# Kernel optimization log

Hardware: AMD Instinct MI355X
Metric: run time of the kernel (lower is better)

Reference implementation:

```python
import jax, jax.numpy as jnp
import numpy as np

N, H, V = 4096, 1024, 16384


def setup_inputs() -> dict:
    key = jax.random.key(0)
    k1, k2, k3, k4 = jax.random.split(key, 4)
    _input = jax.random.normal(k1, (N, H), dtype=jnp.float32)
    weight = jax.random.normal(k2, (V, H), dtype=jnp.float32) * (1.0 / np.sqrt(H))
    target = jax.random.normal(k3, (N, V), dtype=jnp.float32)
    bias = jax.random.normal(k4, (V,), dtype=jnp.float32)
    return {"_input": _input, "weight": weight, "target": target, "bias": bias}


def reference(_input, weight, target, bias):
    # Fused linear + MSE with reduction='mean':
    # logits = _input @ weight.T + bias  -> (N, V)
    # loss = mean((logits - target)**2) over all N*V elements
    logits = jnp.einsum("nh,vh->nv", _input, weight) + bias
    diff = logits - target
    return jnp.mean(diff * diff)
```

## Files before the change

### kernel.cpp

```cpp
#include <hip/hip_runtime.h>
#include <hip/hip_bf16.h>
#include <stdint.h>

#define N_ 4096
#define H_ 1024
#define V_ 16384

using i32x8  = __attribute__((ext_vector_type(8))) int;
using f32x16 = __attribute__((ext_vector_type(16))) float;

__global__ void cast2_f32_to_fp8(const float* __restrict__ in0, uint8_t* __restrict__ out0,
                                 const float* __restrict__ in1, uint8_t* __restrict__ out1,
                                 int nblk0) {
    const float* in;
    uint8_t* out;
    int bid;
    if (blockIdx.x < (unsigned)nblk0) { in = in0; out = out0; bid = blockIdx.x; }
    else                              { in = in1; out = out1; bid = blockIdx.x - nblk0; }
    size_t i = ((size_t)bid * blockDim.x + threadIdx.x) * 8;
    float4 a = *(const float4*)(in + i);
    float4 b = *(const float4*)(in + i + 4);
    int lo = __builtin_amdgcn_cvt_pk_fp8_f32(a.x, a.y, 0, 0);
    lo     = __builtin_amdgcn_cvt_pk_fp8_f32(a.z, a.w, lo, 1);
    int hi = __builtin_amdgcn_cvt_pk_fp8_f32(b.x, b.y, 0, 0);
    hi     = __builtin_amdgcn_cvt_pk_fp8_f32(b.z, b.w, hi, 1);
    *(int2*)(out + i) = make_int2(lo, hi);
}

#define BM 128
#define BN 128
#define BK 64

__global__ __launch_bounds__(256, 4) void gemm_mse(
    const uint8_t* __restrict__ A8,
    const uint8_t* __restrict__ W8,
    const float*  __restrict__ target,
    const float*  __restrict__ bias,
    float* __restrict__ partials)
{
    __shared__ __align__(16) uint8_t As[2][8192];
    __shared__ __align__(16) uint8_t Bs[2][8192];
    __shared__ float red[4];

    const int tid  = threadIdx.x;
    const int w    = tid >> 6;
    const int lane = tid & 63;
    const int l32  = lane & 31;
    const int half = lane >> 5;
    const int wm   = w >> 1;
    const int wn   = w & 1;

    const int flat = blockIdx.x;
    const int xcd  = flat & 7;
    const int idx  = flat >> 3;
    const int tx   = xcd * 16 + (idx & 15);
    const int ty   = idx >> 4;

    const int rowBase = ty * BM;
    const int colBase = tx * BN;

    f32x16 acc[2][2];
#pragma unroll
    for (int i = 0; i < 2; ++i)
#pragma unroll
        for (int j = 0; j < 2; ++j)
#pragma unroll
            for (int r = 0; r < 16; ++r) acc[i][j][r] = 0.f;

    const int ldrow = lane >> 2;
    const int ldkq  = (lane & 3) ^ ((ldrow + (ldrow >> 2)) & 3);

    const int rl  = lane & 15;
    const int rcb = (lane >> 4) & 1;
    const int fl  = (rl + (rl >> 2)) & 3;
    int aOff[2][2], bOff[2][2];
#pragma unroll
    for (int i = 0; i < 2; ++i)
#pragma unroll
        for (int c = 0; c < 2; ++c) {
            const int slot = rl * 4 + (((half << 1) + c) ^ fl);
            aOff[i][c] = ((wm * 2 + i) * 2 + rcb) * 1024 + slot * 16;
            bOff[i][c] = ((wn * 2 + i) * 2 + rcb) * 1024 + slot * 16;
        }

    float biasj[2];
#pragma unroll
    for (int j = 0; j < 2; ++j) biasj[j] = bias[colBase + wn * 64 + j * 32 + l32];

    auto STAGE = [&](int t, int buf) {
        const int kT = t * BK;
#pragma unroll
        for (int c = 0; c < 2; ++c) {
            const int cid  = w * 2 + c;
            const int kOff = kT + ldkq * 16;
            const uint8_t* ga = A8 + (size_t)(rowBase + cid * 16 + ldrow) * H_ + kOff;
            __builtin_amdgcn_global_load_lds(
                (const __attribute__((address_space(1))) void*)ga,
                (__attribute__((address_space(3))) void*)(&As[buf][0] + cid * 1024),
                16, 0, 0);
            const uint8_t* gb = W8 + (size_t)(colBase + cid * 16 + ldrow) * H_ + kOff;
            __builtin_amdgcn_global_load_lds(
                (const __attribute__((address_space(1))) void*)gb,
                (__attribute__((address_space(3))) void*)(&Bs[buf][0] + cid * 1024),
                16, 0, 0);
        }
    };

    STAGE(0, 0);
    asm volatile("s_waitcnt vmcnt(0)" ::: "memory");
    __builtin_amdgcn_s_barrier();
    asm volatile("" ::: "memory");

    int cur = 0;
    for (int t = 0; t < 16; ++t) {
        if (t < 15) STAGE(t + 1, cur ^ 1);
        asm volatile("" ::: "memory");

        const uint8_t* aB = &As[cur][0];
        const uint8_t* bB = &Bs[cur][0];
        i32x8 af[2], bq[2];
#pragma unroll
        for (int i = 0; i < 2; ++i) {
            int4 a0 = *(const int4*)(aB + aOff[i][0]);
            int4 a1 = *(const int4*)(aB + aOff[i][1]);
            af[i][0] = a0.x; af[i][1] = a0.y; af[i][2] = a0.z; af[i][3] = a0.w;
            af[i][4] = a1.x; af[i][5] = a1.y; af[i][6] = a1.z; af[i][7] = a1.w;
            int4 b0 = *(const int4*)(bB + bOff[i][0]);
            int4 b1 = *(const int4*)(bB + bOff[i][1]);
            bq[i][0] = b0.x; bq[i][1] = b0.y; bq[i][2] = b0.z; bq[i][3] = b0.w;
            bq[i][4] = b1.x; bq[i][5] = b1.y; bq[i][6] = b1.z; bq[i][7] = b1.w;
        }
        __builtin_amdgcn_s_setprio(1);
#pragma unroll
        for (int i = 0; i < 2; ++i)
#pragma unroll
            for (int j = 0; j < 2; ++j)
                acc[i][j] = __builtin_amdgcn_mfma_scale_f32_32x32x64_f8f6f4(
                    af[i], bq[j], acc[i][j],
                    0 , 0 ,
                    0, 0x7F7F7F7F,
                    0, 0x7F7F7F7F);
        __builtin_amdgcn_s_setprio(0);

        if (t < 15) {
            asm volatile("s_waitcnt vmcnt(0)" ::: "memory");
            __builtin_amdgcn_s_barrier();
            asm volatile("" ::: "memory");
        }
        cur ^= 1;
    }

    float sum = 0.f;
#pragma unroll
    for (int i = 0; i < 2; ++i) {
#pragma unroll
        for (int r = 0; r < 16; ++r) {
            const int row = (r & 3) + 8 * (r >> 2) + 4 * half;
            const int gm = rowBase + wm * 64 + i * 32 + row;
            const float* trow = target + (size_t)gm * V_ + colBase + wn * 64 + l32;
#pragma unroll
            for (int j = 0; j < 2; ++j) {
                float d = acc[i][j][r] + biasj[j] - trow[j * 32];
                sum += d * d;
            }
        }
    }

#pragma unroll
    for (int off = 32; off; off >>= 1) sum += __shfl_down(sum, off, 64);
    if (lane == 0) red[w] = sum;
    __syncthreads();
    if (tid == 0)
        partials[flat] = red[0] + red[1] + red[2] + red[3];
}

__global__ void finalize_kernel(const float* __restrict__ partials, float* __restrict__ out, int n) {
    float s = 0.f;
    for (int i = threadIdx.x; i < n; i += 256) s += partials[i];
#pragma unroll
    for (int off = 32; off; off >>= 1) s += __shfl_down(s, off, 64);
    __shared__ float red[4];
    const int w = threadIdx.x >> 6, lane = threadIdx.x & 63;
    if (lane == 0) red[w] = s;
    __syncthreads();
    if (threadIdx.x == 0)
        out[0] = (red[0] + red[1] + red[2] + red[3]) * (1.0f / ((float)N_ * (float)V_));
}

extern "C" void kernel_launch(void* const* d_in, const int* in_sizes, int n_in,
                              void* d_out, int out_size, void* d_ws, size_t ws_size,
                              hipStream_t stream) {
    const float* input  = (const float*)d_in[0];
    const float* weight = (const float*)d_in[1];
    const float* target = (const float*)d_in[2];
    const float* bias   = (const float*)d_in[3];
    float* out = (float*)d_out;

    uint8_t* A8 = (uint8_t*)d_ws;
    uint8_t* W8 = A8 + (size_t)N_ * H_;
    float* partials = (float*)(W8 + (size_t)V_ * H_);

    const int nblk0 = (N_ * H_) / (256 * 8);
    const int nblk1 = (V_ * H_) / (256 * 8);
    cast2_f32_to_fp8<<<nblk0 + nblk1, 256, 0, stream>>>(input, A8, weight, W8, nblk0);

    const int nblocks = (V_ / BN) * (N_ / BM);
    gemm_mse<<<nblocks, 256, 0, stream>>>(A8, W8, target, bias, partials);

    finalize_kernel<<<1, 256, 0, stream>>>(partials, out, nblocks);
}
```

Baseline: 455.7 us.

## Deepen GEMM LDS pipeline to four stages with three tiles in flight

Replaces the double-buffered K loop with a four-buffer pipeline that keeps three global-to-LDS tile loads in flight, waiting only for the oldest via partial vmcnt counts. The goal is to hide global memory latency behind the MFMA work. LDS per block doubles to 64KB and the occupancy hint drops from 4 to 2 blocks per CU, so fewer waves are available to hide latency in other ways. Each iteration now has two barriers instead of one.

```diff
diff --git a/kernel.cpp b/kernel.cpp
--- a/kernel.cpp
+++ b/kernel.cpp
@@ -31,15 +31,15 @@
 #define BN 128
 #define BK 64
 
-__global__ __launch_bounds__(256, 4) void gemm_mse(
+__global__ __launch_bounds__(256, 2) void gemm_mse(
     const uint8_t* __restrict__ A8,
     const uint8_t* __restrict__ W8,
     const float*  __restrict__ target,
     const float*  __restrict__ bias,
     float* __restrict__ partials)
 {
-    __shared__ __align__(16) uint8_t As[2][8192];
-    __shared__ __align__(16) uint8_t Bs[2][8192];
+    __shared__ __align__(16) uint8_t As[4][8192];
+    __shared__ __align__(16) uint8_t Bs[4][8192];
     __shared__ float red[4];
 
     const int tid  = threadIdx.x;
@@ -106,18 +106,9 @@
         }
     };
 
-    STAGE(0, 0);
-    asm volatile("s_waitcnt vmcnt(0)" ::: "memory");
-    __builtin_amdgcn_s_barrier();
-    asm volatile("" ::: "memory");
-
-    int cur = 0;
-    for (int t = 0; t < 16; ++t) {
-        if (t < 15) STAGE(t + 1, cur ^ 1);
-        asm volatile("" ::: "memory");
-
-        const uint8_t* aB = &As[cur][0];
-        const uint8_t* bB = &Bs[cur][0];
+    auto COMPUTE = [&](int buf) {
+        const uint8_t* aB = &As[buf][0];
+        const uint8_t* bB = &Bs[buf][0];
         i32x8 af[2], bq[2];
 #pragma unroll
         for (int i = 0; i < 2; ++i) {
@@ -141,14 +132,34 @@
                     0, 0x7F7F7F7F,
                     0, 0x7F7F7F7F);
         __builtin_amdgcn_s_setprio(0);
-
-        if (t < 15) {
-            asm volatile("s_waitcnt vmcnt(0)" ::: "memory");
-            __builtin_amdgcn_s_barrier();
-            asm volatile("" ::: "memory");
-        }
-        cur ^= 1;
+    };
+
+    STAGE(0, 0);
+    STAGE(1, 1);
+    STAGE(2, 2);
+
+    for (int t = 0; t < 13; ++t) {
+        STAGE(t + 3, (t + 3) & 3);
+        asm volatile("s_waitcnt vmcnt(12)" ::: "memory");
+        __builtin_amdgcn_sched_barrier(0);
+        __builtin_amdgcn_s_barrier();
+        COMPUTE(t & 3);
+        __builtin_amdgcn_s_barrier();
     }
+    asm volatile("s_waitcnt vmcnt(8)" ::: "memory");
+    __builtin_amdgcn_sched_barrier(0);
+    __builtin_amdgcn_s_barrier();
+    COMPUTE(13 & 3);
+    __builtin_amdgcn_s_barrier();
+    asm volatile("s_waitcnt vmcnt(4)" ::: "memory");
+    __builtin_amdgcn_sched_barrier(0);
+    __builtin_amdgcn_s_barrier();
+    COMPUTE(14 & 3);
+    __builtin_amdgcn_s_barrier();
+    asm volatile("s_waitcnt vmcnt(0)" ::: "memory");
+    __builtin_amdgcn_sched_barrier(0);
+    __builtin_amdgcn_s_barrier();
+    COMPUTE(15 & 3);
 
     float sum = 0.f;
 #pragma unroll
```

Result: slower. 474.9 us (+4.2%).
